# Performance work log

Measured on AMD Instinct MI355X. Metric: run time of the kernel, lower is better.

The kernel has to match this reference:

```python
import jax, jax.numpy as jnp
import numpy as np

NUM_EXPERTS = 8
TOP_K = 2


def setup_inputs() -> dict:
    key = jax.random.key(0)
    ks = jax.random.split(key, 7)
    B, S, H, I, E = 4, 2048, 2048, 2048, NUM_EXPERTS
    sc = 0.02
    return {
        "hidden_states": jax.random.normal(ks[0], (B, S, H), dtype=jnp.float32),
        "gate_w": jax.random.normal(ks[1], (E, H), dtype=jnp.float32) * sc,
        "gate_b": jax.random.normal(ks[2], (E,), dtype=jnp.float32) * sc,
        "w1": jax.random.normal(ks[3], (E, 2 * I, H), dtype=jnp.float32) * sc,
        "b1": jax.random.normal(ks[4], (E, 2 * I), dtype=jnp.float32) * sc,
        "w2": jax.random.normal(ks[5], (E, H, I), dtype=jnp.float32) * sc,
        "b2": jax.random.normal(ks[6], (E, H), dtype=jnp.float32) * sc,
    }


def reference(hidden_states, gate_w, gate_b, w1, b1, w2, b2):
    B, S, H = hidden_states.shape
    x = hidden_states.reshape(-1, H)  # [T, H]
    # Router: gate linear -> top-k -> softmax over the k selected logits
    logits = x @ gate_w.T + gate_b  # [T, E]
    top_vals, top_idx = jax.lax.top_k(logits, TOP_K)  # [T, K]
    routing = jax.nn.softmax(top_vals.astype(jnp.float32), axis=-1).astype(x.dtype)  # [T, K]
    # per-token combine weight for each expert: sum_k routing[t,k] * (sel[t,k]==e)
    out = jnp.zeros_like(x)
    E = w1.shape[0]
    for e in range(E):
        h = x @ w1[e].T + b1[e]  # [T, 2I]
        # interleaved swiglu: view(-1, dim//2, 2) -> glu = even cols, linear = odd cols
        x_glu = h[:, 0::2]
        x_lin = h[:, 1::2]
        y = x_glu * jax.nn.sigmoid(1.702 * x_glu) * (x_lin + 1.0)  # [T, I]
        ye = y @ w2[e].T + b2[e]  # [T, H]
        we = jnp.sum(routing * (top_idx == e), axis=-1)  # [T]
        out = out + ye * we[:, None]
    return out.reshape(B, S, H)
```

## Files before the change

kernel.cpp:

```cpp
#include <hip/hip_runtime.h>
#include <cstdint>
#include <cstddef>

#define T_TOKENS 8192
#define NSLOT (T_TOKENS * 2)
#define HDIM 2048
#define IDIM 2048
#define TWO_I 4096
#define NE 8
#define BM 128
#define BK 32

typedef __attribute__((ext_vector_type(8))) short short8;
typedef __attribute__((ext_vector_type(4))) float f32x4;

__device__ __forceinline__ unsigned short f2bf(float f) {
    union { float f; unsigned int u; } v; v.f = f;
    unsigned int u = v.u;
    u += 0x7fffu + ((u >> 16) & 1u);
    return (unsigned short)(u >> 16);
}

__device__ __forceinline__ void gload_lds16(const unsigned short* g, unsigned short* l) {
    __builtin_amdgcn_global_load_lds(
        (const __attribute__((address_space(1))) unsigned int*)(g),
        (__attribute__((address_space(3))) unsigned int*)(l), 16, 0, 0);
}

__global__ __launch_bounds__(256) void k_gate(const float* __restrict__ x,
                                              const float* __restrict__ gw,
                                              const float* __restrict__ gb,
                                              int* __restrict__ tok_e,
                                              float* __restrict__ tok_w,
                                              int* __restrict__ counts) {
    __shared__ float gwl[NE * HDIM];
    for (int i = threadIdx.x; i < NE * HDIM / 4; i += 256)
        ((float4*)gwl)[i] = ((const float4*)gw)[i];
    __syncthreads();
    int wid = threadIdx.x >> 6, lane = threadIdx.x & 63;
    int gwave = blockIdx.x * 4 + wid;
    for (int t = gwave; t < T_TOKENS; t += 1024) {
        float acc[NE];
#pragma unroll
        for (int e = 0; e < NE; e++) acc[e] = 0.f;
        const float4* xr = (const float4*)(x + (size_t)t * HDIM);
#pragma unroll
        for (int i0 = 0; i0 < HDIM / 4 / 64; i0++) {
            int i = i0 * 64 + lane;
            float4 xv = xr[i];
#pragma unroll
            for (int e = 0; e < NE; e++) {
                float4 gv = ((const float4*)gwl)[e * (HDIM / 4) + i];
                acc[e] += xv.x * gv.x + xv.y * gv.y + xv.z * gv.z + xv.w * gv.w;
            }
        }
#pragma unroll
        for (int e = 0; e < NE; e++) {
#pragma unroll
            for (int off = 32; off; off >>= 1) acc[e] += __shfl_xor(acc[e], off);
        }
        if (lane == 0) {
            float lg[NE];
#pragma unroll
            for (int e = 0; e < NE; e++) lg[e] = acc[e] + gb[e];
            int i0 = 0;
#pragma unroll
            for (int e = 1; e < NE; e++) if (lg[e] > lg[i0]) i0 = e;
            int i1 = (i0 == 0) ? 1 : 0;
#pragma unroll
            for (int e = 0; e < NE; e++) if (e != i0 && lg[e] > lg[i1]) i1 = e;
            float e1 = __expf(lg[i1] - lg[i0]);
            float s = 1.f + e1;
            tok_e[t * 2 + 0] = i0; tok_e[t * 2 + 1] = i1;
            tok_w[t * 2 + 0] = 1.f / s; tok_w[t * 2 + 1] = e1 / s;
            atomicAdd(&counts[i0], 1);
            atomicAdd(&counts[i1], 1);
        }
    }
}

__global__ void k_prefix(const int* __restrict__ counts, int* __restrict__ base,
                         int* __restrict__ tb) {
    if (threadIdx.x == 0) {
        int b = 0, t = 0;
        for (int e = 0; e < NE; e++) {
            base[e] = b; tb[e] = t;
            b += counts[e];
            t += (counts[e] + BM - 1) / BM;
        }
        base[NE] = b; tb[NE] = t;
    }
}

__global__ __launch_bounds__(256) void k_scatter(const int* __restrict__ tok_e,
                                                 const float* __restrict__ tok_w,
                                                 const int* __restrict__ base,
                                                 int* __restrict__ cursor,
                                                 int* __restrict__ slot_tok,
                                                 int* __restrict__ slot_of) {
    int t = blockIdx.x * 256 + threadIdx.x;
    if (t >= T_TOKENS) return;
#pragma unroll
    for (int k = 0; k < 2; k++) {
        int e = tok_e[t * 2 + k];
        int p = atomicAdd(&cursor[e], 1);
        int s = base[e] + p;
        slot_tok[s] = t;
        slot_of[t * 2 + k] = s;
    }
}

__global__ __launch_bounds__(256) void k_convert(const float* __restrict__ src,
                                                 unsigned short* __restrict__ dst) {
    int i = blockIdx.x * 256 + threadIdx.x;
    float4 v = ((const float4*)src)[i];
    union { unsigned short s[4]; uint2 u; } o;
    o.s[0] = f2bf(v.x); o.s[1] = f2bf(v.y); o.s[2] = f2bf(v.z); o.s[3] = f2bf(v.w);
    ((uint2*)dst)[i] = o.u;
}

__global__ __launch_bounds__(256) void k_gemm1(const unsigned short* __restrict__ Xb,
                                               const unsigned short* __restrict__ W1b,
                                               const float* __restrict__ b1,
                                               const int* __restrict__ slot_tok,
                                               const int* __restrict__ base,
                                               const int* __restrict__ tb,
                                               unsigned short* __restrict__ Y) {
    int g = blockIdx.x >> 5;
    int nt = blockIdx.x & 31;
    if (g >= tb[NE]) return;
    int e = 0;
    while (tb[e + 1] <= g) e++;
    int mt = g - tb[e];
    int slot0 = base[e] + mt * BM;
    int mrows = base[e + 1] - base[e] - mt * BM; if (mrows > BM) mrows = BM;

    __shared__ unsigned short Al[BM * BK];
    __shared__ unsigned short Bg[64 * BK];
    __shared__ unsigned short Bq[64 * BK];
    __shared__ int stok[BM];

    int tid = threadIdx.x;
    if (tid < BM) {
        int s = slot0 + tid;
        if (s > NSLOT - 1) s = NSLOT - 1;
        stok[tid] = slot_tok[s];
    }
    __syncthreads();

    int wid = tid >> 6, lane = tid & 63;
    int c0 = nt * 64;
    const size_t eoff = (size_t)e * TWO_I * HDIM;

    const unsigned short* gsrc[4];
    unsigned short* ldst[4];
#pragma unroll
    for (int j = 0; j < 4; j++) {
        int c = (wid * 4 + j) * 64 + lane;
        if (c < 512) {
            int m = c >> 2, kc = c & 3;
            gsrc[j] = Xb + (size_t)stok[m] * HDIM + kc * 8;
            ldst[j] = &Al[c * 8];
        } else if (c < 768) {
            int cb = c - 512, r = cb >> 2, kc = cb & 3;
            gsrc[j] = W1b + eoff + (size_t)(2 * (c0 + r)) * HDIM + kc * 8;
            ldst[j] = &Bg[cb * 8];
        } else {
            int cq = c - 768, r = cq >> 2, kc = cq & 3;
            gsrc[j] = W1b + eoff + (size_t)(2 * (c0 + r) + 1) * HDIM + kc * 8;
            ldst[j] = &Bq[cq * 8];
        }
    }

    int wm = (wid & 1) * 64, wn = (wid >> 1) * 32;
    int arow = lane & 15, akq = (lane >> 4) * 8;

    f32x4 accg[4][2], accl[4][2];
#pragma unroll
    for (int mi = 0; mi < 4; mi++)
#pragma unroll
        for (int ni = 0; ni < 2; ni++) { accg[mi][ni] = (f32x4)0.f; accl[mi][ni] = (f32x4)0.f; }

    for (int k0 = 0; k0 < HDIM; k0 += BK) {
#pragma unroll
        for (int j = 0; j < 4; j++) gload_lds16(gsrc[j] + k0, ldst[j]);
        __syncthreads();

        short8 af[4];
#pragma unroll
        for (int mi = 0; mi < 4; mi++)
            af[mi] = *(const short8*)&Al[(wm + mi * 16 + arow) * BK + akq];
#pragma unroll
        for (int ni = 0; ni < 2; ni++) {
            short8 bg = *(const short8*)&Bg[(wn + ni * 16 + arow) * BK + akq];
            short8 bl = *(const short8*)&Bq[(wn + ni * 16 + arow) * BK + akq];
#pragma unroll
            for (int mi = 0; mi < 4; mi++) {
                accg[mi][ni] = __builtin_amdgcn_mfma_f32_16x16x32_bf16(af[mi], bg, accg[mi][ni], 0, 0, 0);
                accl[mi][ni] = __builtin_amdgcn_mfma_f32_16x16x32_bf16(af[mi], bl, accl[mi][ni], 0, 0, 0);
            }
        }
        __syncthreads();
    }

    const float* b1e = b1 + (size_t)e * TWO_I;
#pragma unroll
    for (int ni = 0; ni < 2; ni++) {
        int cg = c0 + wn + ni * 16 + arow;
        float bg_ = b1e[2 * cg], bl_ = b1e[2 * cg + 1];
#pragma unroll
        for (int mi = 0; mi < 4; mi++) {
#pragma unroll
            for (int r = 0; r < 4; r++) {
                int m = wm + mi * 16 + (lane >> 4) * 4 + r;
                if (m < mrows) {
                    float gv = accg[mi][ni][r] + bg_;
                    float lv = accl[mi][ni][r] + bl_;
                    float yv = gv * (1.f / (1.f + __expf(-1.702f * gv))) * (lv + 1.f);
                    Y[(size_t)(slot0 + m) * IDIM + cg] = f2bf(yv);
                }
            }
        }
    }
}

__global__ __launch_bounds__(256) void k_gemm2(const unsigned short* __restrict__ Y,
                                               const unsigned short* __restrict__ W2b,
                                               const float* __restrict__ b2,
                                               const int* __restrict__ base,
                                               const int* __restrict__ tb,
                                               float* __restrict__ Y2) {
    int g = blockIdx.x >> 4;
    int nt = blockIdx.x & 15;
    if (g >= tb[NE]) return;
    int e = 0;
    while (tb[e + 1] <= g) e++;
    int mt = g - tb[e];
    int slot0 = base[e] + mt * BM;
    int mrows = base[e + 1] - base[e] - mt * BM; if (mrows > BM) mrows = BM;

    __shared__ unsigned short Al[BM * BK];
    __shared__ unsigned short Bl[BM * BK];

    int tid = threadIdx.x;
    int wid = tid >> 6, lane = tid & 63;
    const size_t eoff = (size_t)e * HDIM * IDIM;

    const unsigned short* gsrc[4];
    unsigned short* ldst[4];
#pragma unroll
    for (int j = 0; j < 4; j++) {
        int c = (wid * 4 + j) * 64 + lane;
        if (c < 512) {
            int m = c >> 2, kc = c & 3;
            int s = slot0 + m; if (s > NSLOT - 1) s = NSLOT - 1;
            gsrc[j] = Y + (size_t)s * IDIM + kc * 8;
            ldst[j] = &Al[c * 8];
        } else {
            int cb = c - 512, r = cb >> 2, kc = cb & 3;
            gsrc[j] = W2b + eoff + (size_t)(nt * 128 + r) * IDIM + kc * 8;
            ldst[j] = &Bl[cb * 8];
        }
    }

    int wm = (wid & 1) * 64, wn = (wid >> 1) * 64;
    int arow = lane & 15, akq = (lane >> 4) * 8;

    f32x4 acc[4][4];
#pragma unroll
    for (int mi = 0; mi < 4; mi++)
#pragma unroll
        for (int ni = 0; ni < 4; ni++) acc[mi][ni] = (f32x4)0.f;

    for (int k0 = 0; k0 < IDIM; k0 += BK) {
#pragma unroll
        for (int j = 0; j < 4; j++) gload_lds16(gsrc[j] + k0, ldst[j]);
        __syncthreads();

        short8 af[4], bf[4];
#pragma unroll
        for (int mi = 0; mi < 4; mi++)
            af[mi] = *(const short8*)&Al[(wm + mi * 16 + arow) * BK + akq];
#pragma unroll
        for (int ni = 0; ni < 4; ni++)
            bf[ni] = *(const short8*)&Bl[(wn + ni * 16 + arow) * BK + akq];
#pragma unroll
        for (int mi = 0; mi < 4; mi++)
#pragma unroll
            for (int ni = 0; ni < 4; ni++)
                acc[mi][ni] = __builtin_amdgcn_mfma_f32_16x16x32_bf16(af[mi], bf[ni], acc[mi][ni], 0, 0, 0);
        __syncthreads();
    }

    const float* b2e = b2 + (size_t)e * HDIM;
#pragma unroll
    for (int ni = 0; ni < 4; ni++) {
        int col = nt * 128 + wn + ni * 16 + arow;
        float bv = b2e[col];
#pragma unroll
        for (int mi = 0; mi < 4; mi++) {
#pragma unroll
            for (int r = 0; r < 4; r++) {
                int m = wm + mi * 16 + (lane >> 4) * 4 + r;
                if (m < mrows)
                    Y2[(size_t)(slot0 + m) * HDIM + col] = acc[mi][ni][r] + bv;
            }
        }
    }
}

__global__ __launch_bounds__(256) void k_combine(const float* __restrict__ Y2,
                                                 const int* __restrict__ slot_of,
                                                 const float* __restrict__ tok_w,
                                                 float* __restrict__ out) {
    int t = blockIdx.x;
    int s0 = slot_of[t * 2], s1 = slot_of[t * 2 + 1];
    float w0 = tok_w[t * 2], w1 = tok_w[t * 2 + 1];
    const float4* r0 = (const float4*)(Y2 + (size_t)s0 * HDIM);
    const float4* r1 = (const float4*)(Y2 + (size_t)s1 * HDIM);
    float4* o = (float4*)(out + (size_t)t * HDIM);
#pragma unroll
    for (int it = 0; it < HDIM / 4 / 256; it++) {
        int i = it * 256 + threadIdx.x;
        float4 a = r0[i], b = r1[i];
        float4 v;
        v.x = w0 * a.x + w1 * b.x;
        v.y = w0 * a.y + w1 * b.y;
        v.z = w0 * a.z + w1 * b.z;
        v.w = w0 * a.w + w1 * b.w;
        o[i] = v;
    }
}

extern "C" void kernel_launch(void* const* d_in, const int* in_sizes, int n_in,
                              void* d_out, int out_size, void* d_ws, size_t ws_size,
                              hipStream_t stream) {
    const float* x  = (const float*)d_in[0];
    const float* gw = (const float*)d_in[1];
    const float* gb = (const float*)d_in[2];
    const float* w1 = (const float*)d_in[3];
    const float* b1 = (const float*)d_in[4];
    const float* w2 = (const float*)d_in[5];
    const float* b2 = (const float*)d_in[6];
    float* out = (float*)d_out;

    char* w = (char*)d_ws;
    int* counts = (int*)w;
    int* cursor = counts + 8;
    int* base   = counts + 16;
    int* tb     = counts + 32;
    int* tok_e    = (int*)(w + 4096);
    float* tok_w  = (float*)(w + 4096 + 65536);
    int* slot_tok = (int*)(w + 4096 + 131072);
    int* slot_of  = (int*)(w + 4096 + 196608);

    size_t off = 1 << 20;
    unsigned short* Xb  = (unsigned short*)(w + off); off += (size_t)T_TOKENS * HDIM * 2;
    unsigned short* Y   = (unsigned short*)(w + off); off += (size_t)NSLOT * IDIM * 2;
    unsigned short* W1b = (unsigned short*)(w + off); off += (size_t)NE * TWO_I * HDIM * 2;
    unsigned short* W2b = (unsigned short*)(w + off); off += (size_t)NE * HDIM * IDIM * 2;
    float*          Y2  = (float*)(w + off);          off += (size_t)NSLOT * HDIM * 4;

    hipMemsetAsync(d_ws, 0, 256, stream);

    hipLaunchKernelGGL(k_gate, dim3(256), dim3(256), 0, stream, x, gw, gb, tok_e, tok_w, counts);
    hipLaunchKernelGGL(k_convert, dim3(T_TOKENS * HDIM / 4 / 256), dim3(256), 0, stream, x, Xb);
    hipLaunchKernelGGL(k_convert, dim3(NE * TWO_I * HDIM / 4 / 256), dim3(256), 0, stream, w1, W1b);
    hipLaunchKernelGGL(k_convert, dim3(NE * HDIM * IDIM / 4 / 256), dim3(256), 0, stream, w2, W2b);
    hipLaunchKernelGGL(k_prefix, dim3(1), dim3(64), 0, stream, counts, base, tb);
    hipLaunchKernelGGL(k_scatter, dim3(T_TOKENS / 256), dim3(256), 0, stream,
                       tok_e, tok_w, base, cursor, slot_tok, slot_of);
    hipLaunchKernelGGL(k_gemm1, dim3(135 * 32), dim3(256), 0, stream,
                       Xb, W1b, b1, slot_tok, base, tb, Y);
    hipLaunchKernelGGL(k_gemm2, dim3(135 * 16), dim3(256), 0, stream,
                       Y, W2b, b2, base, tb, Y2);
    hipLaunchKernelGGL(k_combine, dim3(T_TOKENS), dim3(256), 0, stream,
                       Y2, slot_of, tok_w, out);
}
```

Measured before the change: 1.415 ms.

## Rewrite MoE GEMMs with 256x256 tiles, double-buffered LDS and swizzle

Both expert GEMMs move to 512-thread blocks with 256-row by 256-column tiles, BK=64, and double-buffered LDS filled by direct global-to-LDS loads. Explicit vmcnt waits keep the next stage's loads in flight while MFMAs run on the current buffer. The LDS layout is XOR-swizzled to cut bank conflicts, and setprio raises priority around the MFMA bursts. This is meant to raise arithmetic intensity and hide memory latency, at the cost of higher LDS and register pressure, more padding waste on partial expert tiles, and a fixed MAXTILE grid bound that must cover the per-expert tile count.

```diff
diff --git a/kernel.cpp b/kernel.cpp
--- a/kernel.cpp
+++ b/kernel.cpp
@@ -8,8 +8,10 @@
 #define IDIM 2048
 #define TWO_I 4096
 #define NE 8
-#define BM 128
-#define BK 32
+#define BMG 256
+#define BKG 64
+#define NTK 32
+#define MAXTILE 72
 
 typedef __attribute__((ext_vector_type(8))) short short8;
 typedef __attribute__((ext_vector_type(4))) float f32x4;
@@ -26,6 +28,11 @@
         (const __attribute__((address_space(1))) unsigned int*)(g),
         (__attribute__((address_space(3))) unsigned int*)(l), 16, 0, 0);
 }
+
+#define LGKM0() do { asm volatile("s_waitcnt lgkmcnt(0)" ::: "memory"); __builtin_amdgcn_sched_barrier(0); } while (0)
+#define VM8()   do { asm volatile("s_waitcnt vmcnt(8)"   ::: "memory"); __builtin_amdgcn_sched_barrier(0); } while (0)
+#define VM0()   do { asm volatile("s_waitcnt vmcnt(0)"   ::: "memory"); __builtin_amdgcn_sched_barrier(0); } while (0)
+#define BAR()   __builtin_amdgcn_s_barrier()
 
 __global__ __launch_bounds__(256) void k_gate(const float* __restrict__ x,
                                               const float* __restrict__ gw,
@@ -86,7 +93,7 @@
         for (int e = 0; e < NE; e++) {
             base[e] = b; tb[e] = t;
             b += counts[e];
-            t += (counts[e] + BM - 1) / BM;
+            t += (counts[e] + BMG - 1) / BMG;
         }
         base[NE] = b; tb[NE] = t;
     }
@@ -119,189 +126,254 @@
     ((uint2*)dst)[i] = o.u;
 }
 
-__global__ __launch_bounds__(256) void k_gemm1(const unsigned short* __restrict__ Xb,
-                                               const unsigned short* __restrict__ W1b,
-                                               const float* __restrict__ b1,
-                                               const int* __restrict__ slot_tok,
-                                               const int* __restrict__ base,
-                                               const int* __restrict__ tb,
-                                               unsigned short* __restrict__ Y) {
-    int g = blockIdx.x >> 5;
-    int nt = blockIdx.x & 31;
-    if (g >= tb[NE]) return;
-    int e = 0;
-    while (tb[e + 1] <= g) e++;
-    int mt = g - tb[e];
-    int slot0 = base[e] + mt * BM;
-    int mrows = base[e + 1] - base[e] - mt * BM; if (mrows > BM) mrows = BM;
-
-    __shared__ unsigned short Al[BM * BK];
-    __shared__ unsigned short Bg[64 * BK];
-    __shared__ unsigned short Bq[64 * BK];
-    __shared__ int stok[BM];
-
-    int tid = threadIdx.x;
-    if (tid < BM) {
-        int s = slot0 + tid;
-        if (s > NSLOT - 1) s = NSLOT - 1;
-        stok[tid] = slot_tok[s];
-    }
-    __syncthreads();
-
-    int wid = tid >> 6, lane = tid & 63;
-    int c0 = nt * 64;
-    const size_t eoff = (size_t)e * TWO_I * HDIM;
-
-    const unsigned short* gsrc[4];
-    unsigned short* ldst[4];
-#pragma unroll
-    for (int j = 0; j < 4; j++) {
-        int c = (wid * 4 + j) * 64 + lane;
-        if (c < 512) {
-            int m = c >> 2, kc = c & 3;
-            gsrc[j] = Xb + (size_t)stok[m] * HDIM + kc * 8;
-            ldst[j] = &Al[c * 8];
-        } else if (c < 768) {
-            int cb = c - 512, r = cb >> 2, kc = cb & 3;
-            gsrc[j] = W1b + eoff + (size_t)(2 * (c0 + r)) * HDIM + kc * 8;
-            ldst[j] = &Bg[cb * 8];
-        } else {
-            int cq = c - 768, r = cq >> 2, kc = cq & 3;
-            gsrc[j] = W1b + eoff + (size_t)(2 * (c0 + r) + 1) * HDIM + kc * 8;
-            ldst[j] = &Bq[cq * 8];
-        }
-    }
-
-    int wm = (wid & 1) * 64, wn = (wid >> 1) * 32;
-    int arow = lane & 15, akq = (lane >> 4) * 8;
-
-    f32x4 accg[4][2], accl[4][2];
-#pragma unroll
-    for (int mi = 0; mi < 4; mi++)
-#pragma unroll
-        for (int ni = 0; ni < 2; ni++) { accg[mi][ni] = (f32x4)0.f; accl[mi][ni] = (f32x4)0.f; }
-
-    for (int k0 = 0; k0 < HDIM; k0 += BK) {
-#pragma unroll
-        for (int j = 0; j < 4; j++) gload_lds16(gsrc[j] + k0, ldst[j]);
-        __syncthreads();
-
-        short8 af[4];
-#pragma unroll
-        for (int mi = 0; mi < 4; mi++)
-            af[mi] = *(const short8*)&Al[(wm + mi * 16 + arow) * BK + akq];
-#pragma unroll
-        for (int ni = 0; ni < 2; ni++) {
-            short8 bg = *(const short8*)&Bg[(wn + ni * 16 + arow) * BK + akq];
-            short8 bl = *(const short8*)&Bq[(wn + ni * 16 + arow) * BK + akq];
-#pragma unroll
-            for (int mi = 0; mi < 4; mi++) {
-                accg[mi][ni] = __builtin_amdgcn_mfma_f32_16x16x32_bf16(af[mi], bg, accg[mi][ni], 0, 0, 0);
-                accl[mi][ni] = __builtin_amdgcn_mfma_f32_16x16x32_bf16(af[mi], bl, accl[mi][ni], 0, 0, 0);
-            }
-        }
-        __syncthreads();
-    }
-
-    const float* b1e = b1 + (size_t)e * TWO_I;
-#pragma unroll
-    for (int ni = 0; ni < 2; ni++) {
-        int cg = c0 + wn + ni * 16 + arow;
-        float bg_ = b1e[2 * cg], bl_ = b1e[2 * cg + 1];
-#pragma unroll
-        for (int mi = 0; mi < 4; mi++) {
-#pragma unroll
-            for (int r = 0; r < 4; r++) {
-                int m = wm + mi * 16 + (lane >> 4) * 4 + r;
-                if (m < mrows) {
-                    float gv = accg[mi][ni][r] + bg_;
-                    float lv = accl[mi][ni][r] + bl_;
-                    float yv = gv * (1.f / (1.f + __expf(-1.702f * gv))) * (lv + 1.f);
-                    Y[(size_t)(slot0 + m) * IDIM + cg] = f2bf(yv);
-                }
-            }
-        }
-    }
-}
-
-__global__ __launch_bounds__(256) void k_gemm2(const unsigned short* __restrict__ Y,
-                                               const unsigned short* __restrict__ W2b,
-                                               const float* __restrict__ b2,
-                                               const int* __restrict__ base,
-                                               const int* __restrict__ tb,
-                                               float* __restrict__ Y2) {
+__global__ __launch_bounds__(512, 2) void k_gemm1(const unsigned short* __restrict__ Xb,
+                                                  const unsigned short* __restrict__ W1b,
+                                                  const float* __restrict__ b1,
+                                                  const int* __restrict__ slot_tok,
+                                                  const int* __restrict__ base,
+                                                  const int* __restrict__ tb,
+                                                  unsigned short* __restrict__ Y) {
     int g = blockIdx.x >> 4;
     int nt = blockIdx.x & 15;
     if (g >= tb[NE]) return;
     int e = 0;
     while (tb[e + 1] <= g) e++;
     int mt = g - tb[e];
-    int slot0 = base[e] + mt * BM;
-    int mrows = base[e + 1] - base[e] - mt * BM; if (mrows > BM) mrows = BM;
-
-    __shared__ unsigned short Al[BM * BK];
-    __shared__ unsigned short Bl[BM * BK];
+    int slot0 = base[e] + mt * BMG;
+    int mrows = base[e + 1] - base[e] - mt * BMG; if (mrows > BMG) mrows = BMG;
+
+    __shared__ unsigned short As[2][BMG * BKG];
+    __shared__ unsigned short Bs[2][BMG * BKG];
+    __shared__ int stok[BMG];
+
+    int tid = threadIdx.x;
+    if (tid < BMG) {
+        int s = slot0 + tid; if (s > NSLOT - 1) s = NSLOT - 1;
+        stok[tid] = slot_tok[s];
+    }
+    __syncthreads();
+
+    int wid = tid >> 6, lane = tid & 63;
+    int c0 = nt * 128;
+    const unsigned short* W1e = W1b + (size_t)e * TWO_I * HDIM;
+
+    int srow = tid >> 3;
+    int scp = ((tid & 7) ^ (srow & 7)) * 8;
+    unsigned int gaoff[4], gboff[4];
+#pragma unroll
+    for (int j = 0; j < 4; j++) {
+        int row = j * 64 + srow;
+        gaoff[j] = (unsigned int)stok[row] * HDIM + scp;
+        int wcp = row >> 6, lr = row & 63, q = lr >> 5, idx = lr & 31;
+        int w1r = 2 * (c0 + 32 * wcp + idx) + q;
+        gboff[j] = (unsigned int)w1r * HDIM + scp;
+    }
+    unsigned short* laA = &As[0][tid * 8];
+    unsigned short* laB = &Bs[0][tid * 8];
+
+    auto STAGE = [&](int cbuf, int kk) {
+#pragma unroll
+        for (int j = 0; j < 4; j++)
+            gload_lds16(Xb + gaoff[j] + kk, laA + cbuf * (BMG * BKG) + j * 4096);
+#pragma unroll
+        for (int j = 0; j < 4; j++)
+            gload_lds16(W1e + gboff[j] + kk, laB + cbuf * (BMG * BKG) + j * 4096);
+    };
+
+    int wr = wid & 1, wc = wid >> 1;
+    int fr = lane & 15, kq = lane >> 4;
+    int f7 = fr & 7;
+    int aoff0 = (wr * 128 + fr) * BKG + ((0 + kq) ^ f7) * 8;
+    int aoff1 = (wr * 128 + fr) * BKG + ((4 + kq) ^ f7) * 8;
+    int boff0 = (wc * 64 + fr) * BKG + ((0 + kq) ^ f7) * 8;
+    int boff1 = (wc * 64 + fr) * BKG + ((4 + kq) ^ f7) * 8;
+
+    f32x4 acc[8][4];
+#pragma unroll
+    for (int mi = 0; mi < 8; mi++)
+#pragma unroll
+        for (int ni = 0; ni < 4; ni++) acc[mi][ni] = (f32x4)0.f;
+
+    STAGE(0, 0);
+    STAGE(1, BKG);
+    VM8(); BAR();
+
+    for (int t = 0; t < NTK; t++) {
+        int cb = t & 1;
+        const unsigned short* Ac = &As[0][0] + cb * (BMG * BKG);
+        const unsigned short* Bc = &Bs[0][0] + cb * (BMG * BKG);
+
+        short8 a0[8], bb0[4];
+#pragma unroll
+        for (int mi = 0; mi < 8; mi++) a0[mi] = *(const short8*)(Ac + aoff0 + mi * (16 * BKG));
+#pragma unroll
+        for (int ni = 0; ni < 4; ni++) bb0[ni] = *(const short8*)(Bc + boff0 + ni * (16 * BKG));
+        __builtin_amdgcn_s_setprio(1);
+#pragma unroll
+        for (int mi = 0; mi < 8; mi++)
+#pragma unroll
+            for (int ni = 0; ni < 4; ni++)
+                acc[mi][ni] = __builtin_amdgcn_mfma_f32_16x16x32_bf16(a0[mi], bb0[ni], acc[mi][ni], 0, 0, 0);
+        __builtin_amdgcn_s_setprio(0);
+
+        short8 a1[8], bb1[4];
+#pragma unroll
+        for (int mi = 0; mi < 8; mi++) a1[mi] = *(const short8*)(Ac + aoff1 + mi * (16 * BKG));
+#pragma unroll
+        for (int ni = 0; ni < 4; ni++) bb1[ni] = *(const short8*)(Bc + boff1 + ni * (16 * BKG));
+        LGKM0();
+        BAR();
+        if (t + 2 < NTK) {
+            STAGE(cb, (t + 2) * BKG);
+            VM8();
+        } else {
+            VM0();
+        }
+        __builtin_amdgcn_s_setprio(1);
+#pragma unroll
+        for (int mi = 0; mi < 8; mi++)
+#pragma unroll
+            for (int ni = 0; ni < 4; ni++)
+                acc[mi][ni] = __builtin_amdgcn_mfma_f32_16x16x32_bf16(a1[mi], bb1[ni], acc[mi][ni], 0, 0, 0);
+        __builtin_amdgcn_s_setprio(0);
+        BAR();
+    }
+
+    const float* b1e = b1 + (size_t)e * TWO_I;
+#pragma unroll
+    for (int ni = 0; ni < 2; ni++) {
+        int ycol = c0 + wc * 32 + ni * 16 + fr;
+        float bg_ = b1e[2 * ycol], bl_ = b1e[2 * ycol + 1];
+#pragma unroll
+        for (int mi = 0; mi < 8; mi++) {
+#pragma unroll
+            for (int r = 0; r < 4; r++) {
+                int m = wr * 128 + mi * 16 + kq * 4 + r;
+                if (m < mrows) {
+                    float gv = acc[mi][ni][r] + bg_;
+                    float lv = acc[mi][ni + 2][r] + bl_;
+                    float yv = gv * (1.f / (1.f + __expf(-1.702f * gv))) * (lv + 1.f);
+                    Y[(size_t)(slot0 + m) * IDIM + ycol] = f2bf(yv);
+                }
+            }
+        }
+    }
+}
+
+__global__ __launch_bounds__(512, 2) void k_gemm2(const unsigned short* __restrict__ Y,
+                                                  const unsigned short* __restrict__ W2b,
+                                                  const float* __restrict__ b2,
+                                                  const int* __restrict__ base,
+                                                  const int* __restrict__ tb,
+                                                  float* __restrict__ Y2) {
+    int g = blockIdx.x >> 3;
+    int nt = blockIdx.x & 7;
+    if (g >= tb[NE]) return;
+    int e = 0;
+    while (tb[e + 1] <= g) e++;
+    int mt = g - tb[e];
+    int slot0 = base[e] + mt * BMG;
+    int mrows = base[e + 1] - base[e] - mt * BMG; if (mrows > BMG) mrows = BMG;
+
+    __shared__ unsigned short As[2][BMG * BKG];
+    __shared__ unsigned short Bs[2][BMG * BKG];
 
     int tid = threadIdx.x;
     int wid = tid >> 6, lane = tid & 63;
-    const size_t eoff = (size_t)e * HDIM * IDIM;
-
-    const unsigned short* gsrc[4];
-    unsigned short* ldst[4];
+    int n0 = nt * 256;
+    const unsigned short* W2e = W2b + (size_t)e * HDIM * IDIM;
+
+    int srow = tid >> 3;
+    int scp = ((tid & 7) ^ (srow & 7)) * 8;
+    unsigned int gaoff[4], gboff[4];
 #pragma unroll
     for (int j = 0; j < 4; j++) {
-        int c = (wid * 4 + j) * 64 + lane;
-        if (c < 512) {
-            int m = c >> 2, kc = c & 3;
-            int s = slot0 + m; if (s > NSLOT - 1) s = NSLOT - 1;
-            gsrc[j] = Y + (size_t)s * IDIM + kc * 8;
-            ldst[j] = &Al[c * 8];
+        int row = j * 64 + srow;
+        int s = slot0 + row; if (s > NSLOT - 1) s = NSLOT - 1;
+        gaoff[j] = (unsigned int)s * IDIM + scp;
+        gboff[j] = (unsigned int)(n0 + row) * IDIM + scp;
+    }
+    unsigned short* laA = &As[0][tid * 8];
+    unsigned short* laB = &Bs[0][tid * 8];
+
+    auto STAGE = [&](int cbuf, int kk) {
+#pragma unroll
+        for (int j = 0; j < 4; j++)
+            gload_lds16(Y + gaoff[j] + kk, laA + cbuf * (BMG * BKG) + j * 4096);
+#pragma unroll
+        for (int j = 0; j < 4; j++)
+            gload_lds16(W2e + gboff[j] + kk, laB + cbuf * (BMG * BKG) + j * 4096);
+    };
+
+    int wr = wid & 1, wc = wid >> 1;
+    int fr = lane & 15, kq = lane >> 4;
+    int f7 = fr & 7;
+    int aoff0 = (wr * 128 + fr) * BKG + ((0 + kq) ^ f7) * 8;
+    int aoff1 = (wr * 128 + fr) * BKG + ((4 + kq) ^ f7) * 8;
+    int boff0 = (wc * 64 + fr) * BKG + ((0 + kq) ^ f7) * 8;
+    int boff1 = (wc * 64 + fr) * BKG + ((4 + kq) ^ f7) * 8;
+
+    f32x4 acc[8][4];
+#pragma unroll
+    for (int mi = 0; mi < 8; mi++)
+#pragma unroll
+        for (int ni = 0; ni < 4; ni++) acc[mi][ni] = (f32x4)0.f;
+
+    STAGE(0, 0);
+    STAGE(1, BKG);
+    VM8(); BAR();
+
+    for (int t = 0; t < NTK; t++) {
+        int cb = t & 1;
+        const unsigned short* Ac = &As[0][0] + cb * (BMG * BKG);
+        const unsigned short* Bc = &Bs[0][0] + cb * (BMG * BKG);
+
+        short8 a0[8], bb0[4];
+#pragma unroll
+        for (int mi = 0; mi < 8; mi++) a0[mi] = *(const short8*)(Ac + aoff0 + mi * (16 * BKG));
+#pragma unroll
+        for (int ni = 0; ni < 4; ni++) bb0[ni] = *(const short8*)(Bc + boff0 + ni * (16 * BKG));
+        __builtin_amdgcn_s_setprio(1);
+#pragma unroll
+        for (int mi = 0; mi < 8; mi++)
+#pragma unroll
+            for (int ni = 0; ni < 4; ni++)
+                acc[mi][ni] = __builtin_amdgcn_mfma_f32_16x16x32_bf16(a0[mi], bb0[ni], acc[mi][ni], 0, 0, 0);
+        __builtin_amdgcn_s_setprio(0);
+
+        short8 a1[8], bb1[4];
+#pragma unroll
+        for (int mi = 0; mi < 8; mi++) a1[mi] = *(const short8*)(Ac + aoff1 + mi * (16 * BKG));
+#pragma unroll
+        for (int ni = 0; ni < 4; ni++) bb1[ni] = *(const short8*)(Bc + boff1 + ni * (16 * BKG));
+        LGKM0();
+        BAR();
+        if (t + 2 < NTK) {
+            STAGE(cb, (t + 2) * BKG);
+            VM8();
         } else {
-            int cb = c - 512, r = cb >> 2, kc = cb & 3;
-            gsrc[j] = W2b + eoff + (size_t)(nt * 128 + r) * IDIM + kc * 8;
-            ldst[j] = &Bl[cb * 8];
-        }
-    }
-
-    int wm = (wid & 1) * 64, wn = (wid >> 1) * 64;
-    int arow = lane & 15, akq = (lane >> 4) * 8;
-
-    f32x4 acc[4][4];
-#pragma unroll
-    for (int mi = 0; mi < 4; mi++)
-#pragma unroll
-        for (int ni = 0; ni < 4; ni++) acc[mi][ni] = (f32x4)0.f;
-
-    for (int k0 = 0; k0 < IDIM; k0 += BK) {
-#pragma unroll
-        for (int j = 0; j < 4; j++) gload_lds16(gsrc[j] + k0, ldst[j]);
-        __syncthreads();
-
-        short8 af[4], bf[4];
-#pragma unroll
-        for (int mi = 0; mi < 4; mi++)
-            af[mi] = *(const short8*)&Al[(wm + mi * 16 + arow) * BK + akq];
-#pragma unroll
-        for (int ni = 0; ni < 4; ni++)
-            bf[ni] = *(const short8*)&Bl[(wn + ni * 16 + arow) * BK + akq];
-#pragma unroll
-        for (int mi = 0; mi < 4; mi++)
+            VM0();
+        }
+        __builtin_amdgcn_s_setprio(1);
+#pragma unroll
+        for (int mi = 0; mi < 8; mi++)
 #pragma unroll
             for (int ni = 0; ni < 4; ni++)
-                acc[mi][ni] = __builtin_amdgcn_mfma_f32_16x16x32_bf16(af[mi], bf[ni], acc[mi][ni], 0, 0, 0);
-        __syncthreads();
+                acc[mi][ni] = __builtin_amdgcn_mfma_f32_16x16x32_bf16(a1[mi], bb1[ni], acc[mi][ni], 0, 0, 0);
+        __builtin_amdgcn_s_setprio(0);
+        BAR();
     }
 
     const float* b2e = b2 + (size_t)e * HDIM;
 #pragma unroll
     for (int ni = 0; ni < 4; ni++) {
-        int col = nt * 128 + wn + ni * 16 + arow;
+        int col = n0 + wc * 64 + ni * 16 + fr;
         float bv = b2e[col];
 #pragma unroll
-        for (int mi = 0; mi < 4; mi++) {
+        for (int mi = 0; mi < 8; mi++) {
 #pragma unroll
             for (int r = 0; r < 4; r++) {
-                int m = wm + mi * 16 + (lane >> 4) * 4 + r;
+                int m = wr * 128 + mi * 16 + kq * 4 + r;
                 if (m < mrows)
                     Y2[(size_t)(slot0 + m) * HDIM + col] = acc[mi][ni][r] + bv;
             }
@@ -370,9 +442,9 @@
     hipLaunchKernelGGL(k_prefix, dim3(1), dim3(64), 0, stream, counts, base, tb);
     hipLaunchKernelGGL(k_scatter, dim3(T_TOKENS / 256), dim3(256), 0, stream,
                        tok_e, tok_w, base, cursor, slot_tok, slot_of);
-    hipLaunchKernelGGL(k_gemm1, dim3(135 * 32), dim3(256), 0, stream,
+    hipLaunchKernelGGL(k_gemm1, dim3(MAXTILE * 16), dim3(512), 0, stream,
                        Xb, W1b, b1, slot_tok, base, tb, Y);
-    hipLaunchKernelGGL(k_gemm2, dim3(135 * 16), dim3(256), 0, stream,
+    hipLaunchKernelGGL(k_gemm2, dim3(MAXTILE * 8), dim3(512), 0, stream,
                        Y, W2b, b2, base, tb, Y2);
     hipLaunchKernelGGL(k_combine, dim3(T_TOKENS), dim3(256), 0, stream,
                        Y2, slot_of, tok_w, out);
```

Measured after the change: 1.415 ms. Within noise of the previous version (-0.0%).
